# Kernel tuning notes

Hardware: AMD Instinct MI355X
Metric: run time of the kernel (lower is better)

The kernel has to match this reference:

```python
import jax, jax.numpy as jnp
import numpy as np

# Model dims (match init_kwargs)
E = 16            # real experts
Z = 16            # zero experts (identity)
TOP_K = 4
H = 1024          # hidden_size
I = 512           # intermediate_size per expert
T = 4096          # tokens
ROUTED_SCALING = 1.0


def setup_inputs() -> dict:
    key = jax.random.key(0)
    ks = jax.random.split(key, 6)
    s_h = 1.0 / np.sqrt(H)
    s_i = 1.0 / np.sqrt(I)
    return {
        "hidden_states": jax.random.normal(ks[0], (T, H), jnp.float32),
        # router over E + Z total slots (real experts + zero experts)
        "router_weight": jax.random.normal(ks[1], (E + Z, H), jnp.float32) * s_h,
        "e_score_bias": jax.random.normal(ks[2], (E + Z,), jnp.float32) * 0.01,
        # SwiGLU expert weights
        "w_gate": jax.random.normal(ks[3], (E, H, I), jnp.float32) * s_h,
        "w_up": jax.random.normal(ks[4], (E, H, I), jnp.float32) * s_h,
        "w_down": jax.random.normal(ks[5], (E, I, H), jnp.float32) * s_i,
    }


def reference(hidden_states, router_weight, e_score_bias, w_gate, w_up, w_down):
    x = hidden_states  # [T, H]
    # --- Router (float32, router_dtype == 'float32') ---
    logits = jnp.einsum("th,eh->te", x.astype(jnp.float32), router_weight)  # [T, E+Z]
    scores = jax.nn.softmax(logits, axis=-1)
    # top-k selected on bias-corrected scores; weights taken from raw scores,
    # renormalize=False
    _, topk_ids = jax.lax.top_k(scores + e_score_bias[None, :], TOP_K)  # [T, k]
    topk_w = jnp.take_along_axis(scores, topk_ids, axis=-1)             # [T, k]
    # --- Dispatch/combine weights over all E+Z slots ---
    onehot = jax.nn.one_hot(topk_ids, E + Z, dtype=jnp.float32)  # [T, k, E+Z]
    combine = jnp.einsum("tk,tks->ts", topk_w, onehot)           # [T, E+Z]
    cw_real = combine[:, :E].astype(x.dtype)      # [T, E] routed-expert weights
    zero_w = combine[:, E:].sum(-1).astype(x.dtype)  # [T] identity weight sum
    # --- Grouped-expert SwiGLU (dense dispatch reference) ---
    g = jnp.einsum("th,ehi->eti", x, w_gate)   # [E, T, I]
    u = jnp.einsum("th,ehi->eti", x, w_up)     # [E, T, I]
    act = jax.nn.silu(g) * u
    eout = jnp.einsum("eti,eih->eth", act, w_down)  # [E, T, H]
    routed = jnp.einsum("eth,te->th", eout, cw_real)  # [T, H]
    # zero experts: identity contribution (zero_expert_type == 'identity')
    out = routed * ROUTED_SCALING + zero_w[:, None] * x
    return out
```

## Files before the change

kernel.cpp:

```cpp
#include <hip/hip_runtime.h>
#include <stdint.h>

#define T_TOK 4096
#define Hd    1024
#define Id    512
#define NE    16
#define NSLOT 32
#define TOPK  4
#define ECAP  1024
#define MAXT  (NE * (ECAP/128))

typedef __bf16 bf16x8 __attribute__((ext_vector_type(8)));
typedef float  floatx4 __attribute__((ext_vector_type(4)));

#define WAIT_VM(n) asm volatile("s_waitcnt vmcnt(" #n ")" ::: "memory")

static __device__ __forceinline__ void wg_barrier(){
  asm volatile("" ::: "memory");
  __builtin_amdgcn_s_barrier();
  asm volatile("" ::: "memory");
}

static __device__ __forceinline__ unsigned short f2bf(float f){
  unsigned int u = __float_as_uint(f);
  u = u + 0x7fffu + ((u >> 16) & 1u);
  return (unsigned short)(u >> 16);
}

static __device__ __forceinline__ uint32_t bfpack(uint32_t hi_src, uint32_t lo_src){
  return __builtin_amdgcn_perm(hi_src, lo_src, 0x07060302u);
}

static __device__ __forceinline__ void load_lds16(const void* g, void* l){
  __builtin_amdgcn_global_load_lds((const __attribute__((address_space(1))) void*)g,
                                   (__attribute__((address_space(3))) void*)l, 16, 0, 0);
}

__global__ __launch_bounds__(256) void router_kernel(
    const float* __restrict__ x, const float* __restrict__ rw,
    unsigned short* __restrict__ xb, float* __restrict__ logits,
    int* __restrict__ cursors){
  const int tid = threadIdx.x;
  if (blockIdx.x == 0 && tid < NE) cursors[tid] = 0;
  const int lane = tid & 63, sg = tid >> 6;
  const int t0 = blockIdx.x * 8;
  const int l4 = lane * 4;

  float v[64];
  #pragma unroll
  for (int i = 0; i < 64; ++i) v[i] = 0.f;

  #pragma unroll
  for (int c = 0; c < 4; ++c){
    const int h = c * 256 + l4;
    float4 xv[8];
    #pragma unroll
    for (int t = 0; t < 8; ++t)
      xv[t] = *(const float4*)(x + (size_t)(t0 + t) * Hd + h);
    if (sg == 0){
      #pragma unroll
      for (int t = 0; t < 8; ++t){
        ushort4 o;
        o.x = f2bf(xv[t].x); o.y = f2bf(xv[t].y);
        o.z = f2bf(xv[t].z); o.w = f2bf(xv[t].w);
        *(ushort4*)(xb + (size_t)(t0 + t) * Hd + h) = o;
      }
    }
    #pragma unroll
    for (int s = 0; s < 8; ++s){
      float4 rv = *(const float4*)(rw + (size_t)(sg * 8 + s) * Hd + h);
      #pragma unroll
      for (int t = 0; t < 8; ++t)
        v[t*8 + s] += xv[t].x*rv.x + xv[t].y*rv.y + xv[t].z*rv.z + xv[t].w*rv.w;
    }
  }

  #pragma unroll
  for (int off = 1; off < 64; off <<= 1){
    #pragma unroll
    for (int i = 0; i < 64; i += 2*off){
      const int j = i + off;
      float send  = (lane & off) ? v[i] : v[j];
      float other = __shfl_xor(send, off);
      v[i] = ((lane & off) ? v[j] : v[i]) + other;
    }
  }
  logits[(size_t)(t0 + (lane >> 3)) * NSLOT + sg * 8 + (lane & 7)] = v[0];
}

__global__ __launch_bounds__(256) void transpose_kernel(
    const float* __restrict__ wg, const float* __restrict__ wu,
    const float* __restrict__ wd,
    unsigned short* __restrict__ wgb, unsigned short* __restrict__ wub,
    unsigned short* __restrict__ wdb){
  const int tb = blockIdx.x;
  const int tid = threadIdx.x;
  const float* src; unsigned short* dst; int R, C, rt, ct;
  const int arr = tb >> 10;
  const int rem = tb & 1023;
  const int e  = rem >> 6;
  const int t2 = rem & 63;
  if (arr == 0)      { src = wg; dst = wgb; R = Hd; C = Id; rt = t2 >> 3; ct = t2 & 7;  }
  else if (arr == 1) { src = wu; dst = wub; R = Hd; C = Id; rt = t2 >> 3; ct = t2 & 7;  }
  else               { src = wd; dst = wdb; R = Id; C = Hd; rt = t2 >> 4; ct = t2 & 15; }
  const int r0 = rt * 128, c0 = ct * 64;
  const float* s = src + (size_t)e * R * C;
  unsigned short* d = dst + (size_t)e * R * C;
  const int r_idx = tid >> 4;
  const int c_idx = tid & 15;
  const int rr = r0 + r_idx * 8;
  const int cc = c0 + c_idx * 4;
  uint4 u[8];
  #pragma unroll
  for (int p = 0; p < 8; ++p)
    u[p] = *(const uint4*)(s + (size_t)(rr + p)*C + cc);
  uint4 o;
  o.x = bfpack(u[1].x, u[0].x); o.y = bfpack(u[3].x, u[2].x);
  o.z = bfpack(u[5].x, u[4].x); o.w = bfpack(u[7].x, u[6].x);
  *(uint4*)(d + (size_t)(cc + 0)*R + rr) = o;
  o.x = bfpack(u[1].y, u[0].y); o.y = bfpack(u[3].y, u[2].y);
  o.z = bfpack(u[5].y, u[4].y); o.w = bfpack(u[7].y, u[6].y);
  *(uint4*)(d + (size_t)(cc + 1)*R + rr) = o;
  o.x = bfpack(u[1].z, u[0].z); o.y = bfpack(u[3].z, u[2].z);
  o.z = bfpack(u[5].z, u[4].z); o.w = bfpack(u[7].z, u[6].z);
  *(uint4*)(d + (size_t)(cc + 2)*R + rr) = o;
  o.x = bfpack(u[1].w, u[0].w); o.y = bfpack(u[3].w, u[2].w);
  o.z = bfpack(u[5].w, u[4].w); o.w = bfpack(u[7].w, u[6].w);
  *(uint4*)(d + (size_t)(cc + 3)*R + rr) = o;
}

__global__ __launch_bounds__(256) void topk_kernel(
    const float* __restrict__ logits, const float* __restrict__ bias,
    const float* __restrict__ x,
    int* __restrict__ cursors, int* __restrict__ rowmap, float* __restrict__ roww,
    float* __restrict__ out){
  __shared__ float szw[8];
  const int tid = threadIdx.x;
  if (tid < 8){
    const int t = blockIdx.x * 8 + tid;
    float sc[32], bsc[32];
    #pragma unroll
    for (int i = 0; i < 32; i += 4){
      float4 v = *(const float4*)(logits + (size_t)t*NSLOT + i);
      sc[i] = v.x; sc[i+1] = v.y; sc[i+2] = v.z; sc[i+3] = v.w;
    }
    float mx = sc[0];
    #pragma unroll
    for (int i = 1; i < 32; ++i) mx = fmaxf(mx, sc[i]);
    float sum = 0.f;
    #pragma unroll
    for (int i = 0; i < 32; ++i){ sc[i] = __expf(sc[i]-mx); sum += sc[i]; }
    float inv = 1.f / sum;
    #pragma unroll
    for (int i = 0; i < 32; ++i){ sc[i] *= inv; bsc[i] = sc[i] + bias[i]; }
    unsigned int chosen = 0;
    float zw = 0.f;
    #pragma unroll
    for (int k = 0; k < TOPK; ++k){
      float bv = -1e30f, bw = 0.f; int best = 0;
      #pragma unroll
      for (int i = 0; i < 32; ++i){
        float v = ((chosen >> i) & 1u) ? -1e30f : bsc[i];
        if (v > bv){ bv = v; best = i; bw = sc[i]; }
      }
      chosen |= (1u << best);
      if (best < NE){
        int pos = atomicAdd(&cursors[best], 1);
        rowmap[best*ECAP + pos] = t;
        roww[best*ECAP + pos]   = bw;
      } else zw += bw;
    }
    szw[tid] = zw;
  }
  __syncthreads();
  const int lane = tid & 63, wid = tid >> 6;
  const size_t base = (size_t)blockIdx.x * 8 * Hd;
  #pragma unroll
  for (int r0 = 0; r0 < 8; r0 += 4){
    int r = r0 + wid;
    float s = szw[r];
    const float4* xs = (const float4*)(x + base + (size_t)r*Hd);
    float4* os = (float4*)(out + base + (size_t)r*Hd);
    #pragma unroll
    for (int q = 0; q < 4; ++q){
      float4 v = xs[lane + q*64];
      float4 o; o.x = v.x*s; o.y = v.y*s; o.z = v.z*s; o.w = v.w*s;
      os[lane + q*64] = o;
    }
  }
}

static __device__ __forceinline__ bool tile_map(const int* __restrict__ counts, int tile,
                                                int& e, int& off, int& ne, int& m0){
  int cumT = 0; e = -1; ne = 0; m0 = 0;
  #pragma unroll
  for (int ee = 0; ee < NE; ++ee){
    int c = counts[ee];
    int nt = (c + 127) >> 7;
    bool here = (e < 0) && (tile < cumT + nt);
    if (here){ e = ee; ne = c; m0 = (tile - cumT) * 128; }
    cumT += nt;
  }
  off = (e >= 0) ? e * ECAP : 0;
  return e >= 0;
}

__global__ __launch_bounds__(256, 2) void gateup_kernel(
    const unsigned short* __restrict__ xb,
    const unsigned short* __restrict__ wgb,
    const unsigned short* __restrict__ wub,
    const int* __restrict__ counts,
    const int* __restrict__ rowmap,
    const float* __restrict__ roww,
    unsigned short* __restrict__ act){
  const int b = blockIdx.x;
  int e, off, ne, m0;
  if (!tile_map(counts, b >> 2, e, off, ne, m0)) return;
  const int n0 = (b & 3) * 128;

  __shared__ unsigned short sA [2][128*32];
  __shared__ unsigned short sBg[2][128*32];
  __shared__ unsigned short sBu[2][128*32];
  __shared__ int sT[128];

  const int tid = threadIdx.x, lane = tid & 63, wid = tid >> 6;
  if (tid < 128){ int r = m0 + tid; sT[tid] = rowmap[off + ((r < ne) ? r : 0)]; }
  __syncthreads();

  const int r_in = lane >> 2, seg = lane & 3;
  const int rt0 = wid*32 + r_in, rt1 = rt0 + 16;
  const size_t wbase = (size_t)e * Id * Hd;

  const unsigned short* pA0 = xb + (size_t)sT[rt0]*Hd + seg*8;
  const unsigned short* pA1 = xb + (size_t)sT[rt1]*Hd + seg*8;
  const unsigned short* pG0 = wgb + wbase + (size_t)(n0+rt0)*Hd + seg*8;
  const unsigned short* pG1 = wgb + wbase + (size_t)(n0+rt1)*Hd + seg*8;
  const unsigned short* pU0 = wub + wbase + (size_t)(n0+rt0)*Hd + seg*8;
  const unsigned short* pU1 = wub + wbase + (size_t)(n0+rt1)*Hd + seg*8;
  const int dA0 = wid*1024, dA1 = wid*1024 + 512;

  floatx4 accg[4][4], accu[4][4];
  #pragma unroll
  for (int i = 0; i < 4; ++i)
    #pragma unroll
    for (int j = 0; j < 4; ++j){
      floatx4 z = {0.f,0.f,0.f,0.f};
      accg[i][j] = z; accu[i][j] = z;
    }
  const int wm = (wid & 1) * 64, wn = (wid >> 1) * 64;
  const int fm = lane & 15, fq = lane >> 4;

  load_lds16(pA0, &sA[0][dA0]);  load_lds16(pA1, &sA[0][dA1]);
  load_lds16(pG0, &sBg[0][dA0]); load_lds16(pG1, &sBg[0][dA1]);
  load_lds16(pU0, &sBu[0][dA0]); load_lds16(pU1, &sBu[0][dA1]);

  #pragma unroll 2
  for (int kit = 0; kit < 32; ++kit){
    const int cur = kit & 1;
    if (kit < 31){
      const int nk = (kit+1)*32;
      const int nb = 1 - cur;
      load_lds16(pA0 + nk, &sA[nb][dA0]);  load_lds16(pA1 + nk, &sA[nb][dA1]);
      load_lds16(pG0 + nk, &sBg[nb][dA0]); load_lds16(pG1 + nk, &sBg[nb][dA1]);
      load_lds16(pU0 + nk, &sBu[nb][dA0]); load_lds16(pU1 + nk, &sBu[nb][dA1]);
      WAIT_VM(6);
    } else {
      WAIT_VM(0);
    }
    wg_barrier();
    bf16x8 av[4], bgv[4], buv[4];
    #pragma unroll
    for (int i = 0; i < 4; ++i)
      av[i] = *(const bf16x8*)(&sA[cur][(wm + i*16 + fm)*32 + fq*8]);
    #pragma unroll
    for (int j = 0; j < 4; ++j){
      bgv[j] = *(const bf16x8*)(&sBg[cur][(wn + j*16 + fm)*32 + fq*8]);
      buv[j] = *(const bf16x8*)(&sBu[cur][(wn + j*16 + fm)*32 + fq*8]);
    }
    #pragma unroll
    for (int i = 0; i < 4; ++i)
      #pragma unroll
      for (int j = 0; j < 4; ++j){
        accg[i][j] = __builtin_amdgcn_mfma_f32_16x16x32_bf16(av[i], bgv[j], accg[i][j], 0, 0, 0);
        accu[i][j] = __builtin_amdgcn_mfma_f32_16x16x32_bf16(av[i], buv[j], accu[i][j], 0, 0, 0);
      }
    wg_barrier();
  }

  #pragma unroll
  for (int i = 0; i < 4; ++i){
    #pragma unroll
    for (int r = 0; r < 4; ++r){
      int row = wm + i*16 + fq*4 + r;
      if (m0 + row < ne){
        float w = roww[off + m0 + row];
        size_t rb = (size_t)(off + m0 + row) * Id + n0;
        #pragma unroll
        for (int j = 0; j < 4; ++j){
          float g = accg[i][j][r];
          float u = accu[i][j][r];
          float a = (g / (1.f + __expf(-g))) * u * w;
          act[rb + wn + j*16 + fm] = f2bf(a);
        }
      }
    }
  }
}

__global__ __launch_bounds__(256, 4) void down_kernel(
    const unsigned short* __restrict__ act,
    const unsigned short* __restrict__ wdb,
    const int* __restrict__ counts,
    const int* __restrict__ rowmap,
    float* __restrict__ out){
  const int b = blockIdx.x;
  int e, off, ne, m0;
  if (!tile_map(counts, b >> 3, e, off, ne, m0)) return;
  const int n0 = (b & 7) * 128;

  __shared__ unsigned short sA[2][128*32];
  __shared__ unsigned short sB[2][128*32];
  __shared__ int sT[128];

  const int tid = threadIdx.x, lane = tid & 63, wid = tid >> 6;
  if (tid < 128){ int r = m0 + tid; sT[tid] = (r < ne) ? rowmap[off + r] : 0; }

  const int r_in = lane >> 2, seg = lane & 3;
  const int rt0 = wid*32 + r_in, rt1 = rt0 + 16;
  const int gr0 = off + ((m0 + rt0 < ne) ? (m0 + rt0) : 0);
  const int gr1 = off + ((m0 + rt1 < ne) ? (m0 + rt1) : 0);
  const size_t wbase = (size_t)e * Hd * Id;
  const unsigned short* pA0 = act + (size_t)gr0*Id + seg*8;
  const unsigned short* pA1 = act + (size_t)gr1*Id + seg*8;
  const unsigned short* pB0 = wdb + wbase + (size_t)(n0+rt0)*Id + seg*8;
  const unsigned short* pB1 = wdb + wbase + (size_t)(n0+rt1)*Id + seg*8;
  const int dA0 = wid*1024, dA1 = wid*1024 + 512;

  floatx4 acc[4][4];
  #pragma unroll
  for (int i = 0; i < 4; ++i)
    #pragma unroll
    for (int j = 0; j < 4; ++j){ floatx4 z = {0.f,0.f,0.f,0.f}; acc[i][j] = z; }
  const int wm = (wid & 1) * 64, wn = (wid >> 1) * 64;
  const int fm = lane & 15, fq = lane >> 4;

  load_lds16(pA0, &sA[0][dA0]); load_lds16(pA1, &sA[0][dA1]);
  load_lds16(pB0, &sB[0][dA0]); load_lds16(pB1, &sB[0][dA1]);

  #pragma unroll 2
  for (int kit = 0; kit < 16; ++kit){
    const int cur = kit & 1;
    if (kit < 15){
      const int nk = (kit+1)*32;
      const int nb = 1 - cur;
      load_lds16(pA0 + nk, &sA[nb][dA0]); load_lds16(pA1 + nk, &sA[nb][dA1]);
      load_lds16(pB0 + nk, &sB[nb][dA0]); load_lds16(pB1 + nk, &sB[nb][dA1]);
      WAIT_VM(4);
    } else {
      WAIT_VM(0);
    }
    wg_barrier();
    bf16x8 av[4], bv[4];
    #pragma unroll
    for (int i = 0; i < 4; ++i) av[i] = *(const bf16x8*)(&sA[cur][(wm + i*16 + fm)*32 + fq*8]);
    #pragma unroll
    for (int j = 0; j < 4; ++j) bv[j] = *(const bf16x8*)(&sB[cur][(wn + j*16 + fm)*32 + fq*8]);
    #pragma unroll
    for (int i = 0; i < 4; ++i)
      #pragma unroll
      for (int j = 0; j < 4; ++j)
        acc[i][j] = __builtin_amdgcn_mfma_f32_16x16x32_bf16(av[i], bv[j], acc[i][j], 0, 0, 0);
    wg_barrier();
  }

  #pragma unroll
  for (int i = 0; i < 4; ++i){
    #pragma unroll
    for (int r = 0; r < 4; ++r){
      int row = wm + i*16 + fq*4 + r;
      if (m0 + row < ne){
        int t = sT[row];
        #pragma unroll
        for (int j = 0; j < 4; ++j)
          atomicAdd(&out[(size_t)t*Hd + n0 + wn + j*16 + fm], acc[i][j][r]);
      }
    }
  }
}

extern "C" void kernel_launch(void* const* d_in, const int* in_sizes, int n_in,
                              void* d_out, int out_size, void* d_ws, size_t ws_size,
                              hipStream_t stream){
  (void)in_sizes; (void)n_in; (void)out_size; (void)ws_size;
  const float* x    = (const float*)d_in[0];
  const float* rw   = (const float*)d_in[1];
  const float* bias = (const float*)d_in[2];
  const float* wg   = (const float*)d_in[3];
  const float* wu   = (const float*)d_in[4];
  const float* wd   = (const float*)d_in[5];
  float* out = (float*)d_out;

  char* ws = (char*)d_ws;
  const size_t WSZ = (size_t)NE * Id * Hd * 2;
  unsigned short* wgb = (unsigned short*)(ws);
  unsigned short* wub = (unsigned short*)(ws + WSZ);
  unsigned short* wdb = (unsigned short*)(ws + 2*WSZ);
  unsigned short* xb  = (unsigned short*)(ws + 3*WSZ);
  unsigned short* act = (unsigned short*)(ws + 3*WSZ + (size_t)T_TOK*Hd*2);
  char* misc = ws + 3*WSZ + (size_t)T_TOK*Hd*2 + (size_t)NE*ECAP*Id*2;

  const size_t LOGB = (size_t)T_TOK * NSLOT * 4;
  float* logits  = (float*)misc;
  int*   cursors = (int*)(misc + LOGB);
  char* p2 = misc + LOGB + 256;
  int*   rowmap = (int*)p2;                     p2 += (size_t)NE*ECAP*4;
  float* roww   = (float*)p2;

  router_kernel<<<T_TOK/8, 256, 0, stream>>>(x, rw, xb, logits, cursors);
  transpose_kernel<<<3072, 256, 0, stream>>>(wg, wu, wd, wgb, wub, wdb);
  topk_kernel<<<T_TOK/8, 256, 0, stream>>>(logits, bias, x, cursors, rowmap, roww, out);
  gateup_kernel<<<MAXT*4, 256, 0, stream>>>(xb, wgb, wub, cursors, rowmap, roww, act);
  down_kernel<<<MAXT*8, 256, 0, stream>>>(act, wdb, cursors, rowmap, out);
}
```

Before: 280.9 us.

## Replace atomic scatter in down projection with bf16 partials and gather-combine kernel

The down-projection kernel now writes per-slot results as bf16 into a partials buffer, reusing the gate-weight workspace region, instead of doing float atomicAdd into the output. A new combine kernel gathers up to four partials per token through a token-to-slot map and adds the identity-expert term. The top-k kernel no longer writes the x-scaled output itself and instead records slot indices and zero-expert weights. This removes atomic contention and the ordering dependency on output, but adds an extra kernel launch, an extra round trip through memory, and bf16 rounding of the partial sums.

After: 268.7 us. -4.3%, faster.

```diff
diff --git a/kernel.cpp b/kernel.cpp
--- a/kernel.cpp
+++ b/kernel.cpp
@@ -25,6 +25,10 @@
   unsigned int u = __float_as_uint(f);
   u = u + 0x7fffu + ((u >> 16) & 1u);
   return (unsigned short)(u >> 16);
+}
+
+static __device__ __forceinline__ float bf2f(unsigned short u){
+  return __uint_as_float((unsigned int)u << 16);
 }
 
 static __device__ __forceinline__ uint32_t bfpack(uint32_t hi_src, uint32_t lo_src){
@@ -131,10 +135,8 @@
 
 __global__ __launch_bounds__(256) void topk_kernel(
     const float* __restrict__ logits, const float* __restrict__ bias,
-    const float* __restrict__ x,
     int* __restrict__ cursors, int* __restrict__ rowmap, float* __restrict__ roww,
-    float* __restrict__ out){
-  __shared__ float szw[8];
+    int* __restrict__ tokslot, float* __restrict__ zwbuf){
   const int tid = threadIdx.x;
   if (tid < 8){
     const int t = blockIdx.x * 8 + tid;
@@ -164,29 +166,16 @@
         if (v > bv){ bv = v; best = i; bw = sc[i]; }
       }
       chosen |= (1u << best);
+      int slot = -1;
       if (best < NE){
         int pos = atomicAdd(&cursors[best], 1);
         rowmap[best*ECAP + pos] = t;
         roww[best*ECAP + pos]   = bw;
+        slot = best*ECAP + pos;
       } else zw += bw;
-    }
-    szw[tid] = zw;
-  }
-  __syncthreads();
-  const int lane = tid & 63, wid = tid >> 6;
-  const size_t base = (size_t)blockIdx.x * 8 * Hd;
-  #pragma unroll
-  for (int r0 = 0; r0 < 8; r0 += 4){
-    int r = r0 + wid;
-    float s = szw[r];
-    const float4* xs = (const float4*)(x + base + (size_t)r*Hd);
-    float4* os = (float4*)(out + base + (size_t)r*Hd);
-    #pragma unroll
-    for (int q = 0; q < 4; ++q){
-      float4 v = xs[lane + q*64];
-      float4 o; o.x = v.x*s; o.y = v.y*s; o.z = v.z*s; o.w = v.w*s;
-      os[lane + q*64] = o;
-    }
+      tokslot[t*TOPK + k] = slot;
+    }
+    zwbuf[t] = zw;
   }
 }
 
@@ -311,8 +300,7 @@
     const unsigned short* __restrict__ act,
     const unsigned short* __restrict__ wdb,
     const int* __restrict__ counts,
-    const int* __restrict__ rowmap,
-    float* __restrict__ out){
+    unsigned short* __restrict__ partials){
   const int b = blockIdx.x;
   int e, off, ne, m0;
   if (!tile_map(counts, b >> 3, e, off, ne, m0)) return;
@@ -320,10 +308,8 @@
 
   __shared__ unsigned short sA[2][128*32];
   __shared__ unsigned short sB[2][128*32];
-  __shared__ int sT[128];
 
   const int tid = threadIdx.x, lane = tid & 63, wid = tid >> 6;
-  if (tid < 128){ int r = m0 + tid; sT[tid] = (r < ne) ? rowmap[off + r] : 0; }
 
   const int r_in = lane >> 2, seg = lane & 3;
   const int rt0 = wid*32 + r_in, rt1 = rt0 + 16;
@@ -379,12 +365,48 @@
     for (int r = 0; r < 4; ++r){
       int row = wm + i*16 + fq*4 + r;
       if (m0 + row < ne){
-        int t = sT[row];
+        size_t pb = (size_t)(off + m0 + row) * Hd + n0;
         #pragma unroll
         for (int j = 0; j < 4; ++j)
-          atomicAdd(&out[(size_t)t*Hd + n0 + wn + j*16 + fm], acc[i][j][r]);
+          partials[pb + wn + j*16 + fm] = f2bf(acc[i][j][r]);
       }
     }
+  }
+}
+
+__global__ __launch_bounds__(256) void combine_kernel(
+    const float* __restrict__ x, const unsigned short* __restrict__ partials,
+    const int* __restrict__ tokslot, const float* __restrict__ zwbuf,
+    float* __restrict__ out){
+  const int tid = threadIdx.x;
+  const int t0 = blockIdx.x * 4;
+  const int c4 = tid * 4;
+  #pragma unroll
+  for (int r = 0; r < 4; ++r){
+    const int t = t0 + r;
+    const float zw = zwbuf[t];
+    const int s0 = tokslot[t*TOPK + 0], s1 = tokslot[t*TOPK + 1];
+    const int s2 = tokslot[t*TOPK + 2], s3 = tokslot[t*TOPK + 3];
+    float4 xv = *(const float4*)(x + (size_t)t*Hd + c4);
+    float4 o;
+    o.x = zw*xv.x; o.y = zw*xv.y; o.z = zw*xv.z; o.w = zw*xv.w;
+    if (s0 >= 0){
+      ushort4 p = *(const ushort4*)(partials + (size_t)s0*Hd + c4);
+      o.x += bf2f(p.x); o.y += bf2f(p.y); o.z += bf2f(p.z); o.w += bf2f(p.w);
+    }
+    if (s1 >= 0){
+      ushort4 p = *(const ushort4*)(partials + (size_t)s1*Hd + c4);
+      o.x += bf2f(p.x); o.y += bf2f(p.y); o.z += bf2f(p.z); o.w += bf2f(p.w);
+    }
+    if (s2 >= 0){
+      ushort4 p = *(const ushort4*)(partials + (size_t)s2*Hd + c4);
+      o.x += bf2f(p.x); o.y += bf2f(p.y); o.z += bf2f(p.z); o.w += bf2f(p.w);
+    }
+    if (s3 >= 0){
+      ushort4 p = *(const ushort4*)(partials + (size_t)s3*Hd + c4);
+      o.x += bf2f(p.x); o.y += bf2f(p.y); o.z += bf2f(p.z); o.w += bf2f(p.w);
+    }
+    *(float4*)(out + (size_t)t*Hd + c4) = o;
   }
 }
 
@@ -409,16 +431,22 @@
   unsigned short* act = (unsigned short*)(ws + 3*WSZ + (size_t)T_TOK*Hd*2);
   char* misc = ws + 3*WSZ + (size_t)T_TOK*Hd*2 + (size_t)NE*ECAP*Id*2;
 
+  unsigned short* partials = (unsigned short*)(ws);
+
   const size_t LOGB = (size_t)T_TOK * NSLOT * 4;
   float* logits  = (float*)misc;
   int*   cursors = (int*)(misc + LOGB);
   char* p2 = misc + LOGB + 256;
-  int*   rowmap = (int*)p2;                     p2 += (size_t)NE*ECAP*4;
-  float* roww   = (float*)p2;
+  int*   rowmap  = (int*)p2;                    p2 += (size_t)NE*ECAP*4;
+  float* roww    = (float*)p2;                  p2 += (size_t)NE*ECAP*4;
+  int*   tokslot = (int*)p2;                    p2 += (size_t)T_TOK*TOPK*4;
+  float* zwbuf   = (float*)p2;
 
   router_kernel<<<T_TOK/8, 256, 0, stream>>>(x, rw, xb, logits, cursors);
   transpose_kernel<<<3072, 256, 0, stream>>>(wg, wu, wd, wgb, wub, wdb);
-  topk_kernel<<<T_TOK/8, 256, 0, stream>>>(logits, bias, x, cursors, rowmap, roww, out);
+  topk_kernel<<<T_TOK/8, 256, 0, stream>>>(logits, bias, cursors, rowmap, roww,
+                                           tokslot, zwbuf);
   gateup_kernel<<<MAXT*4, 256, 0, stream>>>(xb, wgb, wub, cursors, rowmap, roww, act);
-  down_kernel<<<MAXT*8, 256, 0, stream>>>(act, wdb, cursors, rowmap, out);
-}
+  down_kernel<<<MAXT*8, 256, 0, stream>>>(act, wdb, cursors, partials);
+  combine_kernel<<<T_TOK/4, 256, 0, stream>>>(x, partials, tokslot, zwbuf, out);
+}
```
